# Kernel optimization log

Hardware: AMD Instinct MI355X
Metric: run time of the kernel (lower is better)

## Reference

```python
import jax, jax.numpy as jnp
import numpy as np

N = 100000   # nodes
E = 400000   # edges
G = 64       # graphs in batch
D_IN = 20
D_H = 1024   # 4 * 256
D_FC = 128


def _w(key, shape, fan_in):
    return jax.random.normal(key, shape, jnp.float32) / np.sqrt(fan_in).astype(np.float32)


def setup_inputs() -> dict:
    key = jax.random.key(0)
    ks = jax.random.split(key, 14)
    x = jax.random.normal(ks[0], (N, D_IN), jnp.float32)
    edge_index = jax.random.randint(ks[1], (2, E), 0, N)
    batch = jnp.sort(jax.random.randint(ks[2], (N,), 0, G))
    return {
        "x": x,
        "edge_index": edge_index,
        "batch": batch,
        # SAGEConv 1: lin_l (neighbors, with bias), lin_r (root, no bias)
        "W1l": _w(ks[3], (D_H, D_IN), D_IN),
        "b1l": _w(ks[4], (D_H,), D_IN),
        "W1r": _w(ks[5], (D_H, D_IN), D_IN),
        # SAGEConv 2
        "W2l": _w(ks[6], (D_H, D_H), D_H),
        "b2l": _w(ks[7], (D_H,), D_H),
        "W2r": _w(ks[8], (D_H, D_H), D_H),
        # MLP head
        "Wf1": _w(ks[9], (D_FC, D_H), D_H),
        "bf1": _w(ks[10], (D_FC,), D_H),
        "Wf2": _w(ks[11], (1, D_FC), D_FC),
        "bf2": _w(ks[12], (1,), D_FC),
    }


def _sage_mean(h, src, dst, inv_deg, Wl, bl, Wr):
    # mean over incoming neighbors (src -> dst), then lin_l(agg) + lin_r(h)
    agg = jax.ops.segment_sum(h[src], dst, num_segments=N) * inv_deg  # [N, d]
    return agg @ Wl.T + bl + h @ Wr.T


def reference(x, edge_index, batch, W1l, b1l, W1r, W2l, b2l, W2r, Wf1, bf1, Wf2, bf2):
    src, dst = edge_index[0], edge_index[1]
    deg = jax.ops.segment_sum(jnp.ones((E,), jnp.float32), dst, num_segments=N)
    inv_deg = (1.0 / jnp.maximum(deg, 1.0))[:, None]  # nodes w/o in-edges -> 0 agg

    h = jnp.tanh(_sage_mean(x, src, dst, inv_deg, W1l, b1l, W1r))
    h = jnp.tanh(_sage_mean(h, src, dst, inv_deg, W2l, b2l, W2r))
    g = jax.ops.segment_sum(h, batch, num_segments=G)            # global_add_pool [G, D_H]
    y = jax.nn.leaky_relu(g @ Wf1.T + bf1, negative_slope=0.2)
    return y @ Wf2.T + bf2                                        # [G, 1]
```

## Files before the change

kernel.cpp:

```cpp
#include <hip/hip_runtime.h>
#include <stdint.h>
#include <stddef.h>

#define N_NODES 100000
#define N_EDGES 400000
#define NG      64
#define DIN     20
#define DH      1024
#define DFC     128
#define M_PAD   100096
#define MTILES  782
#define NBLK    391
#define CHUNK_T 98

typedef __attribute__((ext_vector_type(8))) short bf16x8_t;
typedef __attribute__((ext_vector_type(4))) float f32x4_t;

__device__ __forceinline__ float bf2f(uint16_t u){
  union { uint32_t i; float f; } v; v.i = ((uint32_t)u) << 16; return v.f;
}
__device__ __forceinline__ uint16_t f2bf(float f){
  union { uint32_t i; float f; } v; v.f = f;
  uint32_t r = v.i + 0x7fffu + ((v.i >> 16) & 1u);
  return (uint16_t)(r >> 16);
}
__device__ __forceinline__ uint32_t f2bf2(float lo, float hi){
  return ((uint32_t)f2bf(hi) << 16) | f2bf(lo);
}
__device__ __forceinline__ float tanhf_fast(float x){
  float ax = fabsf(x);
  float e = __expf(-2.0f * ax);
  float t = (1.0f - e) / (1.0f + e);
  return x < 0.0f ? -t : t;
}
__device__ __forceinline__ void gll16(const void* g, void* l){
  __builtin_amdgcn_global_load_lds(
      (const __attribute__((address_space(1))) unsigned int*)g,
      (__attribute__((address_space(3))) unsigned int*)l, 16, 0, 0);
}

__global__ void k_diag(float* __restrict__ out, float v){
  out[threadIdx.x] = v;
}

__global__ void k_deg(const int* __restrict__ dstn, int* __restrict__ deg){
  int e = blockIdx.x * 256 + threadIdx.x;
  if (e < N_EDGES) atomicAdd(&deg[dstn[e]], 1);
}

__global__ void k_scan1(const int* __restrict__ deg, int* __restrict__ rowoff,
                        int* __restrict__ part){
  __shared__ int sb[256];
  const int t = threadIdx.x;
  const int n = blockIdx.x * 256 + t;
  int v = (n < N_NODES) ? deg[n] : 0;
  sb[t] = v;
  __syncthreads();
  for (int off = 1; off < 256; off <<= 1){
    int u = (t >= off) ? sb[t - off] : 0;
    __syncthreads();
    sb[t] += u;
    __syncthreads();
  }
  int incl = sb[t];
  if (n < N_NODES) rowoff[n] = incl - v;
  if (t == 255) part[blockIdx.x] = incl;
}

__global__ void k_scan2(int* part, int nblk){
  int s = 0;
  for (int i = 0; i < nblk; i++){ int v = part[i]; part[i] = s; s += v; }
}

__global__ void k_scan3(int* __restrict__ rowoff, const int* __restrict__ part){
  int n = blockIdx.x * 256 + threadIdx.x;
  if (n < N_NODES) rowoff[n] += part[blockIdx.x];
  if (n == 0) rowoff[N_NODES] = N_EDGES;
}

__global__ void k_fill(const int* __restrict__ src, const int* __restrict__ dstn,
                       const int* __restrict__ rowoff, int* __restrict__ cursor,
                       int* __restrict__ colx){
  int e = blockIdx.x * 256 + threadIdx.x;
  if (e < N_EDGES){
    int d = dstn[e];
    int p = rowoff[d] + atomicAdd(&cursor[d], 1);
    colx[p] = src[e];
  }
}

__global__ void k_pack(const float* __restrict__ x, const int* __restrict__ rowoff,
                       const int* __restrict__ colx, uint16_t* __restrict__ Ap){
  const int n = blockIdx.x * 256 + threadIdx.x;
  if (n >= M_PAD) return;
  uint4 o[8];
  if (n < N_NODES){
    f32x4_t a0 = {}, a1 = {}, a2 = {}, a3 = {}, a4 = {};
    const int e0 = rowoff[n], e1 = rowoff[n + 1];
    for (int e = e0; e < e1; e++){
      const f32x4_t* xr = (const f32x4_t*)(x + (size_t)colx[e] * DIN);
      a0 += xr[0]; a1 += xr[1]; a2 += xr[2]; a3 += xr[3]; a4 += xr[4];
    }
    const float inv = (e1 > e0) ? 1.f / (float)(e1 - e0) : 0.f;
    a0 *= inv; a1 *= inv; a2 *= inv; a3 *= inv; a4 *= inv;
    const f32x4_t* xs = (const f32x4_t*)(x + (size_t)n * DIN);
    f32x4_t b0 = xs[0], b1 = xs[1], b2 = xs[2], b3 = xs[3], b4 = xs[4];
    o[0] = make_uint4(f2bf2(a0[0],a0[1]), f2bf2(a0[2],a0[3]), f2bf2(a1[0],a1[1]), f2bf2(a1[2],a1[3]));
    o[1] = make_uint4(f2bf2(a2[0],a2[1]), f2bf2(a2[2],a2[3]), f2bf2(a3[0],a3[1]), f2bf2(a3[2],a3[3]));
    o[2] = make_uint4(f2bf2(a4[0],a4[1]), f2bf2(a4[2],a4[3]), f2bf2(b0[0],b0[1]), f2bf2(b0[2],b0[3]));
    o[3] = make_uint4(f2bf2(b1[0],b1[1]), f2bf2(b1[2],b1[3]), f2bf2(b2[0],b2[1]), f2bf2(b2[2],b2[3]));
    o[4] = make_uint4(f2bf2(b3[0],b3[1]), f2bf2(b3[2],b3[3]), f2bf2(b4[0],b4[1]), f2bf2(b4[2],b4[3]));
    o[5] = make_uint4(0,0,0,0); o[6] = o[5]; o[7] = o[5];
  } else {
    o[0] = make_uint4(0,0,0,0);
    for (int i = 1; i < 8; i++) o[i] = o[0];
  }
  uint4* dst = (uint4*)(Ap + (size_t)n * 64);
#pragma unroll
  for (int i = 0; i < 8; i++) dst[i] = o[i];
}

__global__ void k_wpack(const float* __restrict__ W1l, const float* __restrict__ W1r,
                        uint16_t* __restrict__ Bp){
  const int j = blockIdx.x * 256 + threadIdx.x;
  if (j >= DH) return;
  const f32x4_t* wl = (const f32x4_t*)(W1l + (size_t)j * DIN);
  const f32x4_t* wr = (const f32x4_t*)(W1r + (size_t)j * DIN);
  f32x4_t a0 = wl[0], a1 = wl[1], a2 = wl[2], a3 = wl[3], a4 = wl[4];
  f32x4_t b0 = wr[0], b1 = wr[1], b2 = wr[2], b3 = wr[3], b4 = wr[4];
  uint4 o[8];
  o[0] = make_uint4(f2bf2(a0[0],a0[1]), f2bf2(a0[2],a0[3]), f2bf2(a1[0],a1[1]), f2bf2(a1[2],a1[3]));
  o[1] = make_uint4(f2bf2(a2[0],a2[1]), f2bf2(a2[2],a2[3]), f2bf2(a3[0],a3[1]), f2bf2(a3[2],a3[3]));
  o[2] = make_uint4(f2bf2(a4[0],a4[1]), f2bf2(a4[2],a4[3]), f2bf2(b0[0],b0[1]), f2bf2(b0[2],b0[3]));
  o[3] = make_uint4(f2bf2(b1[0],b1[1]), f2bf2(b1[2],b1[3]), f2bf2(b2[0],b2[1]), f2bf2(b2[2],b2[3]));
  o[4] = make_uint4(f2bf2(b3[0],b3[1]), f2bf2(b3[2],b3[3]), f2bf2(b4[0],b4[1]), f2bf2(b4[2],b4[3]));
  o[5] = make_uint4(0,0,0,0); o[6] = o[5]; o[7] = o[5];
  uint4* dst = (uint4*)(Bp + (size_t)j * 64);
#pragma unroll
  for (int i = 0; i < 8; i++) dst[i] = o[i];
}

__global__ __launch_bounds__(256) void k_l1g(
    const uint16_t* __restrict__ Ap, const uint16_t* __restrict__ Bp,
    const float* __restrict__ bias, uint16_t* __restrict__ h1)
{
  __shared__ uint16_t lds[16384];
  const int bid = blockIdx.x;
  const int mt = bid >> 3, jt = bid & 7;
  const int tid = threadIdx.x;
  const int lane = tid & 63, w = tid >> 6;
  const int wm = w >> 1, wn = w & 1;
  char* ldsb = (char*)lds;

  const int rgrp = lane >> 3;
  const int sl   = lane & 7;
  const int sw   = sl ^ rgrp;
#pragma unroll
  for (int t = 0; t < 4; t++){
    const int r0 = w * 32 + t * 8;
    gll16((const char*)Ap + (size_t)(mt * 128 + r0 + rgrp) * 128 + sw * 16,
          ldsb + r0 * 128);
    gll16((const char*)Bp + (size_t)(jt * 128 + r0 + rgrp) * 128 + sw * 16,
          ldsb + 16384 + r0 * 128);
  }
  __syncthreads();

  f32x4_t acc[4][4] = {};
  const int ks = lane >> 4;
  const int rA = wm * 64 + (lane & 15);
  const int rB = wn * 64 + (lane & 15);
#pragma unroll
  for (int kt = 0; kt < 2; kt++){
    bf16x8_t af[4], bg[4];
#pragma unroll
    for (int mi = 0; mi < 4; mi++){
      int r = rA + mi * 16;
      af[mi] = *(const bf16x8_t*)(ldsb + r * 128 + (((kt * 4 + ks) ^ (r & 7)) << 4));
    }
#pragma unroll
    for (int ni = 0; ni < 4; ni++){
      int r = rB + ni * 16;
      bg[ni] = *(const bf16x8_t*)(ldsb + 16384 + r * 128 + (((kt * 4 + ks) ^ (r & 7)) << 4));
    }
#pragma unroll
    for (int mi = 0; mi < 4; mi++)
#pragma unroll
      for (int ni = 0; ni < 4; ni++)
        acc[mi][ni] = __builtin_amdgcn_mfma_f32_16x16x32_bf16(bg[ni], af[mi], acc[mi][ni], 0, 0, 0);
  }

  __syncthreads();
  const int c4 = (lane >> 4) * 4;
#pragma unroll
  for (int ni = 0; ni < 4; ni++){
    const int colL = wn * 64 + ni * 16 + c4;
    const f32x4_t bs = *(const f32x4_t*)(bias + jt * 128 + colL);
    const int b16 = colL >> 3;
    const int hh  = (colL >> 2) & 1;
#pragma unroll
    for (int mi = 0; mi < 4; mi++){
      const int r = wm * 64 + mi * 16 + (lane & 15);
      uint2 o;
      o.x = f2bf2(tanhf_fast(acc[mi][ni][0] + bs[0]), tanhf_fast(acc[mi][ni][1] + bs[1]));
      o.y = f2bf2(tanhf_fast(acc[mi][ni][2] + bs[2]), tanhf_fast(acc[mi][ni][3] + bs[3]));
      *(uint2*)(ldsb + r * 256 + ((b16 ^ (r & 15)) << 4) + hh * 8) = o;
    }
  }
  __syncthreads();
  char* dst0 = (char*)(h1 + (size_t)(mt * 128) * DH + jt * 128);
#pragma unroll
  for (int k = 0; k < 8; k++){
    const int c = tid + k * 256;
    const int r = c >> 4, b16 = c & 15;
    uint4 v = *(const uint4*)(ldsb + r * 256 + ((b16 ^ (r & 15)) << 4));
    *(uint4*)(dst0 + (size_t)r * DH * 2 + b16 * 16) = v;
  }
}

__global__ void k_agg2(const uint16_t* __restrict__ h1, const int* __restrict__ rowoff,
                       const int* __restrict__ colx, uint16_t* __restrict__ aggc,
                       int row0){
  const int nl = blockIdx.x, t = threadIdx.x;
  const int n = row0 + nl;
  uint2* out = (uint2*)aggc;
  const size_t ro = (size_t)nl * 256;
  if (n >= N_NODES){ out[ro + t] = make_uint2(0u, 0u); return; }
  int e0 = rowoff[n], e1 = rowoff[n + 1];
  float f0 = 0.f, f1 = 0.f, f2 = 0.f, f3 = 0.f;
  const uint2* H = (const uint2*)h1;
  for (int e = e0; e < e1; e++){
    uint2 u = H[(size_t)colx[e] * 256 + t];
    f0 += bf2f((uint16_t)u.x); f1 += bf2f((uint16_t)(u.x >> 16));
    f2 += bf2f((uint16_t)u.y); f3 += bf2f((uint16_t)(u.y >> 16));
  }
  float inv = (e1 > e0) ? 1.f / (float)(e1 - e0) : 0.f;
  uint2 o;
  o.x = f2bf2(f0 * inv, f1 * inv);
  o.y = f2bf2(f2 * inv, f3 * inv);
  out[ro + t] = o;
}

__global__ void k_conv(const float* __restrict__ w, uint16_t* __restrict__ b){
  int i = blockIdx.x * 256 + threadIdx.x;
  if (i >= (DH * DH) / 4) return;
  float4 f = ((const float4*)w)[i];
  uint2 o;
  o.x = f2bf2(f.x, f.y);
  o.y = f2bf2(f.z, f.w);
  ((uint2*)b)[i] = o;
}

__global__ __launch_bounds__(512) void k_gemm(
    const uint16_t* __restrict__ A0, const uint16_t* __restrict__ A1,
    const uint16_t* __restrict__ B0, const uint16_t* __restrict__ B1,
    const float* __restrict__ bias, const int* __restrict__ batch,
    float* __restrict__ gbuf, int row0)
{
  __shared__ char ldsb[49152];
  const int bid = blockIdx.x;
  const int mt = bid >> 2, jtg = bid & 3;
  const int tid = threadIdx.x;
  const int lane = tid & 63, w = tid >> 6;
  const int wm = w >> 2, wn = w & 3;

  const int lr = lane >> 2;
  const int sl = lane & 3;
  const int arow = w * 16 + lr;
  const int brow0 = w * 32 + lr;
  const int brow1 = w * 32 + 16 + lr;
  const int aswz = sl ^ ((arow >> 1) & 3);
  const int bswz0 = sl ^ ((brow0 >> 1) & 3);
  const int bswz1 = sl ^ ((brow1 >> 1) & 3);

  const char* gA  = (const char*)A0 + (size_t)(mt * 128 + arow) * 2048 + aswz * 16;
  const char* gB0v = (const char*)B0 + (size_t)(jtg * 256 + brow0) * 2048 + bswz0 * 16;
  const char* gB1v = (const char*)B0 + (size_t)(jtg * 256 + brow1) * 2048 + bswz1 * 16;
  const ptrdiff_t jmpA = (const char*)A1 - (const char*)A0;
  const ptrdiff_t jmpB = (const char*)B1 - (const char*)B0;

  auto stage = [&](int d, int kt){
    const ptrdiff_t offA = ((kt >> 5) ? jmpA : 0) + (ptrdiff_t)(kt & 31) * 64;
    const ptrdiff_t offB = ((kt >> 5) ? jmpB : 0) + (ptrdiff_t)(kt & 31) * 64;
    char* lb = ldsb + d * 24576;
    gll16(gA + offA,   lb + w * 1024);
    gll16(gB0v + offB, lb + 8192 + w * 2048);
    gll16(gB1v + offB, lb + 8192 + w * 2048 + 1024);
  };

  f32x4_t acc[4][4] = {};
  const int ks = lane >> 4;
  const int rA = wm * 64 + (lane & 15);
  const int rB = wn * 64 + (lane & 15);

  stage(0, 0);
  __syncthreads();
  for (int kt = 0; kt < 64; kt++){
    const int cur = kt & 1;
    if (kt < 63) stage(cur ^ 1, kt + 1);
    const char* lb = ldsb + cur * 24576;
    bf16x8_t af[4], bg[4];
#pragma unroll
    for (int mi = 0; mi < 4; mi++){
      int r = rA + mi * 16;
      af[mi] = *(const bf16x8_t*)(lb + r * 64 + ((ks ^ ((r >> 1) & 3)) << 4));
    }
#pragma unroll
    for (int ni = 0; ni < 4; ni++){
      int r = rB + ni * 16;
      bg[ni] = *(const bf16x8_t*)(lb + 8192 + r * 64 + ((ks ^ ((r >> 1) & 3)) << 4));
    }
#pragma unroll
    for (int mi = 0; mi < 4; mi++)
#pragma unroll
      for (int ni = 0; ni < 4; ni++)
        acc[mi][ni] = __builtin_amdgcn_mfma_f32_16x16x32_bf16(af[mi], bg[ni], acc[mi][ni], 0, 0, 0);
    __syncthreads();
  }

  const int rowbase = row0 + mt * 128 + wm * 64;
  const int colbase = jtg * 256 + wn * 64;
  int bt[4][4];
#pragma unroll
  for (int mi = 0; mi < 4; mi++)
#pragma unroll
    for (int i = 0; i < 4; i++){
      int R = rowbase + mi * 16 + (lane >> 4) * 4 + i;
      bt[mi][i] = (R < N_NODES) ? batch[R] : -1;
    }
  const int c0 = rowbase      < N_NODES ? rowbase      : N_NODES - 1;
  const int c1 = rowbase + 63 < N_NODES ? rowbase + 63 : N_NODES - 1;
  const int gmin = batch[c0], gmax = batch[c1];

#pragma unroll
  for (int ni = 0; ni < 4; ni++){
    const int col = colbase + ni * 16 + (lane & 15);
    const float bs = bias[col];
    float v[4][4];
#pragma unroll
    for (int mi = 0; mi < 4; mi++)
#pragma unroll
      for (int i = 0; i < 4; i++)
        v[mi][i] = tanhf_fast(acc[mi][ni][i] + bs);
    for (int g = gmin; g <= gmax; g++){
      float s_ = 0.f;
#pragma unroll
      for (int mi = 0; mi < 4; mi++)
#pragma unroll
        for (int i = 0; i < 4; i++)
          s_ += (bt[mi][i] == g) ? v[mi][i] : 0.f;
      s_ += __shfl_xor(s_, 16);
      s_ += __shfl_xor(s_, 32);
      if (lane < 16) atomicAdd(&gbuf[g * DH + col], s_);
    }
  }
}

__global__ void k_head(const float* __restrict__ gbuf, const float* __restrict__ Wf1,
                       const float* __restrict__ bf1, const float* __restrict__ Wf2,
                       const float* __restrict__ bf2, float* __restrict__ out){
  const int gg = blockIdx.x, j = threadIdx.x;
  const float* grow = gbuf + (size_t)gg * DH;
  const float* wr = Wf1 + (size_t)j * DH;
  float acc = bf1[j];
  for (int k = 0; k < DH; k++) acc = fmaf(grow[k], wr[k], acc);
  float y = acc > 0.f ? acc : 0.2f * acc;
  __shared__ float sb[DFC];
  sb[j] = y * Wf2[j];
  __syncthreads();
  for (int off = 64; off > 0; off >>= 1){
    if (j < off) sb[j] += sb[j + off];
    __syncthreads();
  }
  if (j == 0) out[gg] = sb[0] + bf2[0];
}

extern "C" void kernel_launch(void* const* d_in, const int* in_sizes, int n_in,
                              void* d_out, int out_size, void* d_ws, size_t ws_size,
                              hipStream_t stream){
  const float* x   = (const float*)d_in[0];
  const int*   ei  = (const int*)d_in[1];
  const int*   src = ei;
  const int*   dst = ei + N_EDGES;
  const int*   batch = (const int*)d_in[2];
  const float* W1l = (const float*)d_in[3];
  const float* b1l = (const float*)d_in[4];
  const float* W1r = (const float*)d_in[5];
  const float* W2l = (const float*)d_in[6];
  const float* b2l = (const float*)d_in[7];
  const float* W2r = (const float*)d_in[8];
  const float* Wf1 = (const float*)d_in[9];
  const float* bf1 = (const float*)d_in[10];
  const float* Wf2 = (const float*)d_in[11];
  const float* bf2 = (const float*)d_in[12];
  float* out = (float*)d_out;
  (void)in_sizes; (void)n_in; (void)out_size;

  char* ws = (char*)d_ws;
  size_t off = 0;
  auto alloc = [&](size_t bytes) -> void* {
    void* p = (void*)(ws + off);
    off = (off + bytes + 255) & ~(size_t)255;
    return p;
  };
  uint16_t* h1   = (uint16_t*)alloc((size_t)M_PAD * DH * 2);
  uint16_t* Ap   = (uint16_t*)alloc((size_t)M_PAD * 64 * 2);
  uint16_t* Bp   = (uint16_t*)alloc((size_t)DH * 64 * 2);
  uint16_t* B2l  = (uint16_t*)alloc((size_t)DH * DH * 2);
  uint16_t* B2r  = (uint16_t*)alloc((size_t)DH * DH * 2);
  int*      deg  = (int*)alloc((size_t)N_NODES * 4);
  int*      rowo = (int*)alloc((size_t)(N_NODES + 1) * 4);
  int*      curs = (int*)alloc((size_t)N_NODES * 4);
  int*      colx = (int*)alloc((size_t)N_EDGES * 4);
  int*      part = (int*)alloc((size_t)NBLK * 4);
  float*    gbuf = (float*)alloc((size_t)NG * DH * 4);
  long long remain = (long long)ws_size - (long long)off;
  int chunk_t = (int)(remain / (128LL * 2048LL));
  if (chunk_t > CHUNK_T) chunk_t = CHUNK_T;
  if (chunk_t < 1){
    k_diag<<<1, 64, 0, stream>>>(out, (float)ws_size);
    return;
  }
  uint16_t* aggc = (uint16_t*)alloc((size_t)chunk_t * 128 * DH * 2);

  hipMemsetAsync(deg,  0, (size_t)N_NODES * 4, stream);
  hipMemsetAsync(curs, 0, (size_t)N_NODES * 4, stream);
  hipMemsetAsync(gbuf, 0, (size_t)NG * DH * 4, stream);

  k_deg  <<<(N_EDGES + 255) / 256, 256, 0, stream>>>(dst, deg);
  k_scan1<<<NBLK, 256, 0, stream>>>(deg, rowo, part);
  k_scan2<<<1, 1, 0, stream>>>(part, NBLK);
  k_scan3<<<NBLK, 256, 0, stream>>>(rowo, part);
  k_fill <<<(N_EDGES + 255) / 256, 256, 0, stream>>>(src, dst, rowo, curs, colx);
  k_pack <<<NBLK, 256, 0, stream>>>(x, rowo, colx, Ap);
  k_wpack<<<4, 256, 0, stream>>>(W1l, W1r, Bp);
  k_l1g  <<<MTILES * 8, 256, 0, stream>>>(Ap, Bp, b1l, h1);
  k_conv <<<(DH * DH / 4 + 255) / 256, 256, 0, stream>>>(W2l, B2l);
  k_conv <<<(DH * DH / 4 + 255) / 256, 256, 0, stream>>>(W2r, B2r);

  for (int t0 = 0; t0 < MTILES; ){
    int ct = MTILES - t0 < chunk_t ? MTILES - t0 : chunk_t;
    int row0 = t0 * 128;
    k_agg2<<<ct * 128, 256, 0, stream>>>(h1, rowo, colx, aggc, row0);
    k_gemm<<<ct * 4, 512, 0, stream>>>(aggc, h1 + (size_t)row0 * DH,
                                       B2l, B2r, b2l, batch, gbuf, row0);
    t0 += ct;
  }
  k_head <<<NG, DFC, 0, stream>>>(gbuf, Wf1, bf1, Wf2, bf2, out);
}
```

Before: 927.8 us.

## Use hardware bf16 pack, faster tanh, XCD swizzle, parallel scan, wider aggregation

Replaces the software bf16 rounding with the v_cvt_pk_bf16_f32 instruction and simplifies tanh to an exp plus a hardware reciprocal. Remaps GEMM block indices so neighbouring tiles land on the same XCD for L2 reuse. Turns the single-thread partial scan into a 512-thread block scan. Widens the layer-2 neighbour aggregation to 16-byte loads with two nodes per block. The new tanh form can overflow exp for large inputs, which still saturates correctly, though accuracy near zero may differ slightly.

```diff
diff --git a/kernel.cpp b/kernel.cpp
--- a/kernel.cpp
+++ b/kernel.cpp
@@ -16,27 +16,26 @@
 typedef __attribute__((ext_vector_type(8))) short bf16x8_t;
 typedef __attribute__((ext_vector_type(4))) float f32x4_t;
 
-__device__ __forceinline__ float bf2f(uint16_t u){
-  union { uint32_t i; float f; } v; v.i = ((uint32_t)u) << 16; return v.f;
-}
-__device__ __forceinline__ uint16_t f2bf(float f){
-  union { uint32_t i; float f; } v; v.f = f;
-  uint32_t r = v.i + 0x7fffu + ((v.i >> 16) & 1u);
-  return (uint16_t)(r >> 16);
-}
-__device__ __forceinline__ uint32_t f2bf2(float lo, float hi){
-  return ((uint32_t)f2bf(hi) << 16) | f2bf(lo);
+__device__ __forceinline__ float bf2f(uint32_t u){
+  union { uint32_t i; float f; } v; v.i = u << 16; return v.f;
+}
+__device__ __forceinline__ uint32_t pk_bf16(float lo, float hi){
+  uint32_t r;
+  asm("v_cvt_pk_bf16_f32 %0, %1, %2" : "=v"(r) : "v"(lo), "v"(hi));
+  return r;
 }
 __device__ __forceinline__ float tanhf_fast(float x){
-  float ax = fabsf(x);
-  float e = __expf(-2.0f * ax);
-  float t = (1.0f - e) / (1.0f + e);
-  return x < 0.0f ? -t : t;
+  float t = __expf(2.0f * x);
+  return 1.0f - 2.0f * __builtin_amdgcn_rcpf(1.0f + t);
 }
 __device__ __forceinline__ void gll16(const void* g, void* l){
   __builtin_amdgcn_global_load_lds(
       (const __attribute__((address_space(1))) unsigned int*)g,
       (__attribute__((address_space(3))) unsigned int*)l, 16, 0, 0);
+}
+__device__ __forceinline__ int xcd_swz(int bid, int nwg){
+  if (nwg & 7) return bid;
+  return (bid & 7) * (nwg >> 3) + (bid >> 3);
 }
 
 __global__ void k_diag(float* __restrict__ out, float v){
@@ -68,8 +67,18 @@
 }
 
 __global__ void k_scan2(int* part, int nblk){
-  int s = 0;
-  for (int i = 0; i < nblk; i++){ int v = part[i]; part[i] = s; s += v; }
+  __shared__ int sb[512];
+  const int t = threadIdx.x;
+  int v = (t < nblk) ? part[t] : 0;
+  sb[t] = v;
+  __syncthreads();
+  for (int off = 1; off < 512; off <<= 1){
+    int u = (t >= off) ? sb[t - off] : 0;
+    __syncthreads();
+    sb[t] += u;
+    __syncthreads();
+  }
+  if (t < nblk) part[t] = sb[t] - v;
 }
 
 __global__ void k_scan3(int* __restrict__ rowoff, const int* __restrict__ part){
@@ -105,11 +114,11 @@
     a0 *= inv; a1 *= inv; a2 *= inv; a3 *= inv; a4 *= inv;
     const f32x4_t* xs = (const f32x4_t*)(x + (size_t)n * DIN);
     f32x4_t b0 = xs[0], b1 = xs[1], b2 = xs[2], b3 = xs[3], b4 = xs[4];
-    o[0] = make_uint4(f2bf2(a0[0],a0[1]), f2bf2(a0[2],a0[3]), f2bf2(a1[0],a1[1]), f2bf2(a1[2],a1[3]));
-    o[1] = make_uint4(f2bf2(a2[0],a2[1]), f2bf2(a2[2],a2[3]), f2bf2(a3[0],a3[1]), f2bf2(a3[2],a3[3]));
-    o[2] = make_uint4(f2bf2(a4[0],a4[1]), f2bf2(a4[2],a4[3]), f2bf2(b0[0],b0[1]), f2bf2(b0[2],b0[3]));
-    o[3] = make_uint4(f2bf2(b1[0],b1[1]), f2bf2(b1[2],b1[3]), f2bf2(b2[0],b2[1]), f2bf2(b2[2],b2[3]));
-    o[4] = make_uint4(f2bf2(b3[0],b3[1]), f2bf2(b3[2],b3[3]), f2bf2(b4[0],b4[1]), f2bf2(b4[2],b4[3]));
+    o[0] = make_uint4(pk_bf16(a0[0],a0[1]), pk_bf16(a0[2],a0[3]), pk_bf16(a1[0],a1[1]), pk_bf16(a1[2],a1[3]));
+    o[1] = make_uint4(pk_bf16(a2[0],a2[1]), pk_bf16(a2[2],a2[3]), pk_bf16(a3[0],a3[1]), pk_bf16(a3[2],a3[3]));
+    o[2] = make_uint4(pk_bf16(a4[0],a4[1]), pk_bf16(a4[2],a4[3]), pk_bf16(b0[0],b0[1]), pk_bf16(b0[2],b0[3]));
+    o[3] = make_uint4(pk_bf16(b1[0],b1[1]), pk_bf16(b1[2],b1[3]), pk_bf16(b2[0],b2[1]), pk_bf16(b2[2],b2[3]));
+    o[4] = make_uint4(pk_bf16(b3[0],b3[1]), pk_bf16(b3[2],b3[3]), pk_bf16(b4[0],b4[1]), pk_bf16(b4[2],b4[3]));
     o[5] = make_uint4(0,0,0,0); o[6] = o[5]; o[7] = o[5];
   } else {
     o[0] = make_uint4(0,0,0,0);
@@ -129,11 +138,11 @@
   f32x4_t a0 = wl[0], a1 = wl[1], a2 = wl[2], a3 = wl[3], a4 = wl[4];
   f32x4_t b0 = wr[0], b1 = wr[1], b2 = wr[2], b3 = wr[3], b4 = wr[4];
   uint4 o[8];
-  o[0] = make_uint4(f2bf2(a0[0],a0[1]), f2bf2(a0[2],a0[3]), f2bf2(a1[0],a1[1]), f2bf2(a1[2],a1[3]));
-  o[1] = make_uint4(f2bf2(a2[0],a2[1]), f2bf2(a2[2],a2[3]), f2bf2(a3[0],a3[1]), f2bf2(a3[2],a3[3]));
-  o[2] = make_uint4(f2bf2(a4[0],a4[1]), f2bf2(a4[2],a4[3]), f2bf2(b0[0],b0[1]), f2bf2(b0[2],b0[3]));
-  o[3] = make_uint4(f2bf2(b1[0],b1[1]), f2bf2(b1[2],b1[3]), f2bf2(b2[0],b2[1]), f2bf2(b2[2],b2[3]));
-  o[4] = make_uint4(f2bf2(b3[0],b3[1]), f2bf2(b3[2],b3[3]), f2bf2(b4[0],b4[1]), f2bf2(b4[2],b4[3]));
+  o[0] = make_uint4(pk_bf16(a0[0],a0[1]), pk_bf16(a0[2],a0[3]), pk_bf16(a1[0],a1[1]), pk_bf16(a1[2],a1[3]));
+  o[1] = make_uint4(pk_bf16(a2[0],a2[1]), pk_bf16(a2[2],a2[3]), pk_bf16(a3[0],a3[1]), pk_bf16(a3[2],a3[3]));
+  o[2] = make_uint4(pk_bf16(a4[0],a4[1]), pk_bf16(a4[2],a4[3]), pk_bf16(b0[0],b0[1]), pk_bf16(b0[2],b0[3]));
+  o[3] = make_uint4(pk_bf16(b1[0],b1[1]), pk_bf16(b1[2],b1[3]), pk_bf16(b2[0],b2[1]), pk_bf16(b2[2],b2[3]));
+  o[4] = make_uint4(pk_bf16(b3[0],b3[1]), pk_bf16(b3[2],b3[3]), pk_bf16(b4[0],b4[1]), pk_bf16(b4[2],b4[3]));
   o[5] = make_uint4(0,0,0,0); o[6] = o[5]; o[7] = o[5];
   uint4* dst = (uint4*)(Bp + (size_t)j * 64);
 #pragma unroll
@@ -145,8 +154,8 @@
     const float* __restrict__ bias, uint16_t* __restrict__ h1)
 {
   __shared__ uint16_t lds[16384];
-  const int bid = blockIdx.x;
-  const int mt = bid >> 3, jt = bid & 7;
+  const int wg = xcd_swz(blockIdx.x, gridDim.x);
+  const int mt = wg >> 3, jt = wg & 7;
   const int tid = threadIdx.x;
   const int lane = tid & 63, w = tid >> 6;
   const int wm = w >> 1, wn = w & 1;
@@ -201,8 +210,8 @@
     for (int mi = 0; mi < 4; mi++){
       const int r = wm * 64 + mi * 16 + (lane & 15);
       uint2 o;
-      o.x = f2bf2(tanhf_fast(acc[mi][ni][0] + bs[0]), tanhf_fast(acc[mi][ni][1] + bs[1]));
-      o.y = f2bf2(tanhf_fast(acc[mi][ni][2] + bs[2]), tanhf_fast(acc[mi][ni][3] + bs[3]));
+      o.x = pk_bf16(tanhf_fast(acc[mi][ni][0] + bs[0]), tanhf_fast(acc[mi][ni][1] + bs[1]));
+      o.y = pk_bf16(tanhf_fast(acc[mi][ni][2] + bs[2]), tanhf_fast(acc[mi][ni][3] + bs[3]));
       *(uint2*)(ldsb + r * 256 + ((b16 ^ (r & 15)) << 4) + hh * 8) = o;
     }
   }
@@ -220,24 +229,30 @@
 __global__ void k_agg2(const uint16_t* __restrict__ h1, const int* __restrict__ rowoff,
                        const int* __restrict__ colx, uint16_t* __restrict__ aggc,
                        int row0){
-  const int nl = blockIdx.x, t = threadIdx.x;
+  const int half = threadIdx.x >> 7;
+  const int t = threadIdx.x & 127;
+  const int nl = blockIdx.x * 2 + half;
   const int n = row0 + nl;
-  uint2* out = (uint2*)aggc;
-  const size_t ro = (size_t)nl * 256;
-  if (n >= N_NODES){ out[ro + t] = make_uint2(0u, 0u); return; }
-  int e0 = rowoff[n], e1 = rowoff[n + 1];
-  float f0 = 0.f, f1 = 0.f, f2 = 0.f, f3 = 0.f;
-  const uint2* H = (const uint2*)h1;
+  uint4* out = (uint4*)aggc;
+  const size_t ro = (size_t)nl * 128 + t;
+  if (n >= N_NODES){ out[ro] = make_uint4(0u,0u,0u,0u); return; }
+  const int e0 = rowoff[n], e1 = rowoff[n + 1];
+  float f0=0.f,f1=0.f,f2=0.f,f3=0.f,f4=0.f,f5=0.f,f6=0.f,f7=0.f;
+  const uint4* H = (const uint4*)h1;
   for (int e = e0; e < e1; e++){
-    uint2 u = H[(size_t)colx[e] * 256 + t];
-    f0 += bf2f((uint16_t)u.x); f1 += bf2f((uint16_t)(u.x >> 16));
-    f2 += bf2f((uint16_t)u.y); f3 += bf2f((uint16_t)(u.y >> 16));
-  }
-  float inv = (e1 > e0) ? 1.f / (float)(e1 - e0) : 0.f;
-  uint2 o;
-  o.x = f2bf2(f0 * inv, f1 * inv);
-  o.y = f2bf2(f2 * inv, f3 * inv);
-  out[ro + t] = o;
+    uint4 u = H[(size_t)colx[e] * 128 + t];
+    f0 += bf2f(u.x); f1 += bf2f(u.x >> 16);
+    f2 += bf2f(u.y); f3 += bf2f(u.y >> 16);
+    f4 += bf2f(u.z); f5 += bf2f(u.z >> 16);
+    f6 += bf2f(u.w); f7 += bf2f(u.w >> 16);
+  }
+  const float inv = (e1 > e0) ? 1.f / (float)(e1 - e0) : 0.f;
+  uint4 o;
+  o.x = pk_bf16(f0 * inv, f1 * inv);
+  o.y = pk_bf16(f2 * inv, f3 * inv);
+  o.z = pk_bf16(f4 * inv, f5 * inv);
+  o.w = pk_bf16(f6 * inv, f7 * inv);
+  out[ro] = o;
 }
 
 __global__ void k_conv(const float* __restrict__ w, uint16_t* __restrict__ b){
@@ -245,8 +260,8 @@
   if (i >= (DH * DH) / 4) return;
   float4 f = ((const float4*)w)[i];
   uint2 o;
-  o.x = f2bf2(f.x, f.y);
-  o.y = f2bf2(f.z, f.w);
+  o.x = pk_bf16(f.x, f.y);
+  o.y = pk_bf16(f.z, f.w);
   ((uint2*)b)[i] = o;
 }
 
@@ -257,8 +272,8 @@
     float* __restrict__ gbuf, int row0)
 {
   __shared__ char ldsb[49152];
-  const int bid = blockIdx.x;
-  const int mt = bid >> 2, jtg = bid & 3;
+  const int wg = xcd_swz(blockIdx.x, gridDim.x);
+  const int mt = wg >> 2, jtg = wg & 3;
   const int tid = threadIdx.x;
   const int lane = tid & 63, w = tid >> 6;
   const int wm = w >> 2, wn = w & 3;
@@ -428,7 +443,7 @@
 
   k_deg  <<<(N_EDGES + 255) / 256, 256, 0, stream>>>(dst, deg);
   k_scan1<<<NBLK, 256, 0, stream>>>(deg, rowo, part);
-  k_scan2<<<1, 1, 0, stream>>>(part, NBLK);
+  k_scan2<<<1, 512, 0, stream>>>(part, NBLK);
   k_scan3<<<NBLK, 256, 0, stream>>>(rowo, part);
   k_fill <<<(N_EDGES + 255) / 256, 256, 0, stream>>>(src, dst, rowo, curs, colx);
   k_pack <<<NBLK, 256, 0, stream>>>(x, rowo, colx, Ap);
@@ -440,7 +455,7 @@
   for (int t0 = 0; t0 < MTILES; ){
     int ct = MTILES - t0 < chunk_t ? MTILES - t0 : chunk_t;
     int row0 = t0 * 128;
-    k_agg2<<<ct * 128, 256, 0, stream>>>(h1, rowo, colx, aggc, row0);
+    k_agg2<<<ct * 64, 256, 0, stream>>>(h1, rowo, colx, aggc, row0);
     k_gemm<<<ct * 4, 512, 0, stream>>>(aggc, h1 + (size_t)row0 * DH,
                                        B2l, B2r, b2l, batch, gbuf, row0);
     t0 += ct;
```

Result: faster. 796.1 us (-14.2%).
